# Kernel tuning notes

Measured on AMD Instinct MI355X. Metric: run time of the kernel, lower is better.

The kernel has to match this reference:

```python
import jax, jax.numpy as jnp
import numpy as np

N_HEADS = 16
DIM = 1024
HEAD_DIM = DIM // N_HEADS

def setup_inputs() -> dict:
    key = jax.random.key(0)
    ks = jax.random.split(key, 5)
    x = jax.random.normal(ks[0], (4, 2048, DIM), dtype=jnp.float32)
    W_attn = jax.random.normal(ks[1], (DIM, 3 * DIM), dtype=jnp.float32) / np.sqrt(DIM)
    b_attn = jnp.zeros((3 * DIM,), dtype=jnp.float32)
    W_proj = jax.random.normal(ks[2], (DIM, DIM), dtype=jnp.float32) / np.sqrt(DIM)
    b_proj = jnp.zeros((DIM,), dtype=jnp.float32)
    return {"x": x, "W_attn": W_attn, "b_attn": b_attn, "W_proj": W_proj, "b_proj": b_proj}

def reference(x, W_attn, b_attn, W_proj, b_proj):
    B, S, D = x.shape
    qkv = x @ W_attn + b_attn                      # [B,S,3D]
    q, k, v = jnp.split(qkv, 3, axis=2)
    def heads(t):
        return t.reshape(B, S, N_HEADS, HEAD_DIM).transpose(0, 2, 1, 3)  # [B,H,S,hd]
    qh, kh, vh = heads(q), heads(k), heads(v)
    scale = 1.0 / np.sqrt(HEAD_DIM).astype(np.float32)
    scores = jnp.einsum('bhqd,bhkd->bhqk', qh, kh) * scale  # [B,H,S,S]
    causal = jnp.tril(jnp.ones((S, S), dtype=bool))
    scores = jnp.where(causal, scores, -jnp.inf)
    probs = jax.nn.softmax(scores, axis=-1)
    ctx = jnp.einsum('bhqk,bhkd->bhqd', probs, vh)           # [B,H,S,hd]
    ctx = ctx.transpose(0, 2, 1, 3).reshape(B, S, D)
    return ctx @ W_proj + b_proj
```

## Files before the change

### kernel.cpp

```cpp
#include <hip/hip_runtime.h>
#include <hip/hip_bf16.h>
#include <stdint.h>

typedef __attribute__((ext_vector_type(4))) float  f32x4a;
typedef __attribute__((ext_vector_type(8))) short  bf16x8s;
typedef __attribute__((ext_vector_type(8))) unsigned short u16x8;

#define QSCALE 0.18033688011112042f

static __device__ __forceinline__ unsigned short f2bf(float f) {
    union { float f; uint32_t u; } v; v.f = f;
    uint32_t u = v.u;
    return (unsigned short)((u + 0x7FFFu + ((u >> 16) & 1u)) >> 16);
}

static __device__ __forceinline__ unsigned int pack2bf(float lo, float hi) {
    __hip_bfloat162 t = __float22bfloat162_rn(make_float2(lo, hi));
    union { __hip_bfloat162 b; unsigned int u; } c; c.b = t;
    return c.u;
}

static __device__ __forceinline__ float exp2a(float x) {
    float r;
    asm("v_exp_f32 %0, %1" : "=v"(r) : "v"(x));
    return r;
}

#define GLL(src, dst)                                                          \
    __builtin_amdgcn_global_load_lds(                                          \
        (const __attribute__((address_space(1))) void*)(src),                  \
        (__attribute__((address_space(3))) void*)(dst), 16, 0, 0)

__global__ __launch_bounds__(256) void k_cvt_bf16(const float* __restrict__ in,
                                                  unsigned short* __restrict__ out, int n8) {
    int i = blockIdx.x * blockDim.x + threadIdx.x;
    if (i >= n8) return;
    const float4* p = (const float4*)(in + (size_t)i * 8);
    float4 a = p[0], b = p[1];
    u16x8 o;
    o[0] = f2bf(a.x); o[1] = f2bf(a.y); o[2] = f2bf(a.z); o[3] = f2bf(a.w);
    o[4] = f2bf(b.x); o[5] = f2bf(b.y); o[6] = f2bf(b.z); o[7] = f2bf(b.w);
    *(u16x8*)(out + (size_t)i * 8) = o;
}

__global__ __launch_bounds__(256) void k_transpose_w(const float* __restrict__ W,
                                                     unsigned short* __restrict__ Wt,
                                                     int K, int N, float sc, int nscale) {
    __shared__ float tile[64][68];
    int bx = blockIdx.x;
    int ntn = N >> 6;
    int kt = bx / ntn, nt = bx % ntn;
    int t = threadIdx.x;
    int r0 = t >> 4;
    int c4 = (t & 15) << 2;
    for (int i = 0; i < 4; ++i) {
        int k = r0 + i * 16;
        float4 v = *(const float4*)(W + (size_t)(kt * 64 + k) * N + nt * 64 + c4);
        tile[k][c4 + 0] = v.x; tile[k][c4 + 1] = v.y;
        tile[k][c4 + 2] = v.z; tile[k][c4 + 3] = v.w;
    }
    __syncthreads();
    int nl = t >> 2;
    int kc = (t & 3) << 4;
    float s = (nt * 64 + nl < nscale) ? sc : 1.0f;
    unsigned short* dst = Wt + (size_t)(nt * 64 + nl) * K + kt * 64 + kc;
    u16x8 o0, o1;
    for (int i = 0; i < 8; ++i) o0[i] = f2bf(tile[kc + i][nl] * s);
    for (int i = 0; i < 8; ++i) o1[i] = f2bf(tile[kc + 8 + i][nl] * s);
    *(u16x8*)dst = o0;
    *(u16x8*)(dst + 8) = o1;
}

template<int OUT_BF16, int VW, int QS>
__global__ __launch_bounds__(512, 4) void k_gemm2b(const unsigned short* __restrict__ A,
                                                   const unsigned short* __restrict__ Bt,
                                                   const float* __restrict__ bias,
                                                   void* __restrict__ Cout,
                                                   unsigned short* __restrict__ vt,
                                                   int M, int N, int K, int ntn) {
    __shared__ __align__(16) unsigned short S[3][12288];
    unsigned short* Sf = &S[0][0];

    int nwg = gridDim.x;
    int bid = blockIdx.x;
    int wg = (bid & 7) * (nwg >> 3) + (bid >> 3);
    int mt = wg / ntn, nt = wg % ntn;
    size_t m0 = (size_t)mt * 128, n0 = (size_t)nt * 256;

    int tid = threadIdx.x;
    int w = tid >> 6, lane = tid & 63;
    int wm = w >> 2, wn = w & 3;
    int l15 = lane & 15, l4 = lane >> 4;

    int srow = tid >> 2;
    int sch = (tid & 3) ^ ((srow >> 1) & 3);
    const unsigned short* Asrc = A  + (m0 + srow) * (size_t)K + sch * 8;
    const unsigned short* Bsrc = Bt + (n0 + srow) * (size_t)K + sch * 8;

#define STG(bufoff, kt)                                                                   \
    do {                                                                                  \
        GLL(Asrc + (size_t)(kt) * 32,                    Sf + (bufoff) + tid * 8);        \
        GLL(Bsrc + (size_t)(kt) * 32,                    Sf + (bufoff) + 4096 + tid * 8); \
        GLL(Bsrc + (size_t)(kt) * 32 + (size_t)128 * K,  Sf + (bufoff) + 8192 + tid * 8); \
    } while (0)

    int ck = (l4 ^ ((l15 >> 1) & 3)) * 8;
    int aoff = (wm * 64 + l15) * 32 + ck;
    int boff = 4096 + (wn * 64 + l15) * 32 + ck;

    f32x4a acc[4][4] = {};

#define BAR() __builtin_amdgcn_s_barrier()

    int NT = K >> 5;

    STG(0, 0);
    STG(12288, 1);
    asm volatile("s_waitcnt vmcnt(3)" ::: "memory");
    __builtin_amdgcn_sched_barrier(0);
    BAR();

    int cb = 0;
    for (int t = 0; t < NT; ++t) {
        int sb = cb + 24576; if (sb >= 36864) sb -= 36864;
        bool more = (t + 2) < NT;
        if (more) STG(sb, t + 2);
        bf16x8s af[4], bf[4];
        #pragma unroll
        for (int q = 0; q < 4; ++q) af[q] = *(const bf16x8s*)(Sf + cb + aoff + q * 512);
        #pragma unroll
        for (int q = 0; q < 4; ++q) bf[q] = *(const bf16x8s*)(Sf + cb + boff + q * 512);
        #pragma unroll
        for (int mf = 0; mf < 4; ++mf)
            #pragma unroll
            for (int nf = 0; nf < 4; ++nf)
                acc[mf][nf] = __builtin_amdgcn_mfma_f32_16x16x32_bf16(af[mf], bf[nf],
                                                                      acc[mf][nf], 0, 0, 0);
        if (more) { asm volatile("s_waitcnt vmcnt(3)" ::: "memory"); }
        else      { asm volatile("s_waitcnt vmcnt(0)" ::: "memory"); }
        __builtin_amdgcn_sched_barrier(0);
        BAR();
        cb += 12288; if (cb >= 36864) cb = 0;
    }

    if (VW && nt >= 8) {
        int b = (int)(m0 >> 11);
        int sb_ = ((int)m0 & 2047) + wm * 64;
        #pragma unroll
        for (int nf = 0; nf < 4; ++nf) {
            int vc = ((int)n0 - 2048) + wn * 64 + nf * 16 + l15;
            int h = vc >> 6, d = vc & 63;
            float bv = bias[2048 + vc];
            unsigned short* vrow = vt + ((size_t)(b * 16 + h) * 64 + d) * 2048;
            #pragma unroll
            for (int mf = 0; mf < 4; ++mf) {
                int s = sb_ + mf * 16 + l4 * 4;
                uint2 pv = make_uint2(pack2bf(acc[mf][nf][0] + bv, acc[mf][nf][1] + bv),
                                      pack2bf(acc[mf][nf][2] + bv, acc[mf][nf][3] + bv));
                *(uint2*)(vrow + s) = pv;
            }
        }
    } else {
        #pragma unroll
        for (int nf = 0; nf < 4; ++nf) {
            int col = (int)n0 + wn * 64 + nf * 16 + l15;
            float bv = bias[col];
            if (QS && col < 1024) bv *= QSCALE;
            #pragma unroll
            for (int mf = 0; mf < 4; ++mf) {
                int rbase = (int)m0 + wm * 64 + mf * 16 + l4 * 4;
                #pragma unroll
                for (int rr = 0; rr < 4; ++rr) {
                    float v = acc[mf][nf][rr] + bv;
                    if (OUT_BF16)
                        ((unsigned short*)Cout)[(size_t)(rbase + rr) * N + col] = f2bf(v);
                    else
                        ((float*)Cout)[(size_t)(rbase + rr) * N + col] = v;
                }
            }
        }
    }
#undef STG
#undef BAR
}

__global__ __launch_bounds__(256, 2) void k_attn(const unsigned short* __restrict__ qkv,
                                                 const unsigned short* __restrict__ vt,
                                                 unsigned short* __restrict__ ctx) {
    __shared__ unsigned short Ks[2][8192];
    __shared__ unsigned short Vs[2][8192];
    __shared__ unsigned short Pb[4][2048];
    int bx = blockIdx.x;
    int bh = bx & 63;
    int pr = bx >> 6;
    int b = bh >> 4, hd = bh & 15;
    int tid = threadIdx.x;
    int w = tid >> 6, lane = tid & 63;
    int l15 = lane & 15, l4 = lane >> 4;

    const unsigned short* Qb  = qkv + (size_t)b * 2048 * 3072 + hd * 64;
    const unsigned short* Kb  = Qb + 1024;
    const unsigned short* Vtb = vt + (size_t)bh * 64 * 2048;

    int kr = tid >> 3, kc = tid & 7;
    const unsigned short* Ksr = Kb + (size_t)kr * 3072 + ((kc ^ (kr & 7)) << 3);
    int vr = tid >> 4, vc = tid & 15;
    const unsigned short* Vsr = Vtb + (size_t)vr * 2048 + ((vc ^ (vr & 7)) << 3);
    unsigned short* pbw = &Pb[w][0];

    int psw  = l15 & 7;
    int ph   = (l4 & 1) * 4;
    int pc0  = ((0 + (l4 >> 1)) ^ psw) * 8;
    int pc1  = ((2 + (l4 >> 1)) ^ psw) * 8;
    int pc2  = ((4 + (l4 >> 1)) ^ psw) * 8;
    int pc3  = ((6 + (l4 >> 1)) ^ psw) * 8;
    int pr0  = ((0 + l4) ^ psw) * 8;
    int pr1  = ((4 + l4) ^ psw) * 8;
    int prow0 = l15 * 64;
    int prow1 = (l15 + 16) * 64;

    bf16x8s onesf;
    #pragma unroll
    for (int i = 0; i < 8; ++i) onesf[i] = (short)0x3F80;

#define STAGE(buf, kv0s)                                                                 \
    do {                                                                                 \
        _Pragma("unroll")                                                                \
        for (int i_ = 0; i_ < 4; ++i_)                                                   \
            GLL(Ksr + (size_t)((kv0s) + 32 * i_) * 3072,                                 \
                &Ks[buf][i_ * 2048 + w * 512]);                                          \
        _Pragma("unroll")                                                                \
        for (int i_ = 0; i_ < 4; ++i_)                                                   \
            GLL(Vsr + (size_t)(16 * i_) * 2048 + (kv0s),                                 \
                &Vs[buf][i_ * 2048 + w * 512]);                                          \
    } while (0)

    for (int half = 0; half < 2; ++half) {
        int j = half ? (15 - pr) : pr;
        int q0 = j * 128 + w * 32;
        int qa0 = q0 + l15, qa1 = q0 + 16 + l15;
        bf16x8s qf[2][2];
        {
            const unsigned short* p0 = Qb + (size_t)(q0 + l15) * 3072 + l4 * 8;
            qf[0][0] = *(const bf16x8s*)p0;
            qf[0][1] = *(const bf16x8s*)(p0 + 32);
            const unsigned short* p1 = p0 + (size_t)16 * 3072;
            qf[1][0] = *(const bf16x8s*)p1;
            qf[1][1] = *(const bf16x8s*)(p1 + 32);
        }
        f32x4a o[2][4] = {};
        f32x4a lsum[2] = {};
        const int NT128 = j + 1;

        STAGE(0, 0);
        asm volatile("s_waitcnt vmcnt(0)" ::: "memory");
        __builtin_amdgcn_sched_barrier(0);
        __builtin_amdgcn_s_barrier();

        for (int t = 0; t < NT128; ++t) {
            int cur = t & 1;
            if (t + 1 < NT128) STAGE(cur ^ 1, (t + 1) * 128);

            const unsigned short* Kbuf = Ks[cur];
            const unsigned short* Vbuf = Vs[cur];

            #pragma unroll
            for (int hh2 = 0; hh2 < 2; ++hh2) {
                int kvh = t * 128 + hh2 * 64;
                if (kvh > q0 + 31) continue;

                bf16x8s vf[2][4];
                #pragma unroll
                for (int g = 0; g < 2; ++g)
                    #pragma unroll
                    for (int nf = 0; nf < 4; ++nf) {
                        int rv = nf * 16 + l15;
                        int c  = hh2 * 8 + g * 4 + l4;
                        vf[g][nf] = *(const bf16x8s*)(Vbuf + rv * 128 + ((c ^ (rv & 7)) << 3));
                    }

                f32x4a z[2][4];
                __builtin_amdgcn_s_setprio(1);
                #pragma unroll
                for (int f = 0; f < 4; ++f) {
                    int rk = hh2 * 64 + f * 16 + l15;
                    bf16x8s ka = *(const bf16x8s*)(Kbuf + rk * 64 + ((l4 ^ psw) << 3));
                    bf16x8s kb = *(const bf16x8s*)(Kbuf + rk * 64 + (((4 + l4) ^ psw) << 3));
                    #pragma unroll
                    for (int g = 0; g < 2; ++g) {
                        f32x4a zz = {0.f, 0.f, 0.f, 0.f};
                        zz = __builtin_amdgcn_mfma_f32_16x16x32_bf16(ka, qf[g][0], zz, 0, 0, 0);
                        zz = __builtin_amdgcn_mfma_f32_16x16x32_bf16(kb, qf[g][1], zz, 0, 0, 0);
                        z[g][f] = zz;
                    }
                }
                __builtin_amdgcn_s_setprio(0);

                if (kvh + 63 > q0) {
                    #pragma unroll
                    for (int f = 0; f < 4; ++f)
                        #pragma unroll
                        for (int r = 0; r < 4; ++r) {
                            int kvp = kvh + f * 16 + l4 * 4 + r;
                            if (kvp > qa0) z[0][f][r] = -1e30f;
                            if (kvp > qa1) z[1][f][r] = -1e30f;
                        }
                }

                f32x4a p4[2][4];
                #pragma unroll
                for (int g = 0; g < 2; ++g)
                    #pragma unroll
                    for (int f = 0; f < 4; ++f)
                        #pragma unroll
                        for (int r = 0; r < 4; ++r)
                            p4[g][f][r] = exp2a(z[g][f][r]);

                unsigned int pk[2][8];
                #pragma unroll
                for (int g = 0; g < 2; ++g)
                    #pragma unroll
                    for (int f = 0; f < 4; ++f) {
                        pk[g][2 * f]     = pack2bf(p4[g][f][0], p4[g][f][1]);
                        pk[g][2 * f + 1] = pack2bf(p4[g][f][2], p4[g][f][3]);
                    }

                *(uint2*)(pbw + prow0 + pc0 + ph) = make_uint2(pk[0][0], pk[0][1]);
                *(uint2*)(pbw + prow0 + pc1 + ph) = make_uint2(pk[0][2], pk[0][3]);
                *(uint2*)(pbw + prow0 + pc2 + ph) = make_uint2(pk[0][4], pk[0][5]);
                *(uint2*)(pbw + prow0 + pc3 + ph) = make_uint2(pk[0][6], pk[0][7]);
                *(uint2*)(pbw + prow1 + pc0 + ph) = make_uint2(pk[1][0], pk[1][1]);
                *(uint2*)(pbw + prow1 + pc1 + ph) = make_uint2(pk[1][2], pk[1][3]);
                *(uint2*)(pbw + prow1 + pc2 + ph) = make_uint2(pk[1][4], pk[1][5]);
                *(uint2*)(pbw + prow1 + pc3 + ph) = make_uint2(pk[1][6], pk[1][7]);
                asm volatile("" ::: "memory");
                bf16x8s pa[2][2];
                pa[0][0] = *(const bf16x8s*)(pbw + prow0 + pr0);
                pa[0][1] = *(const bf16x8s*)(pbw + prow0 + pr1);
                pa[1][0] = *(const bf16x8s*)(pbw + prow1 + pr0);
                pa[1][1] = *(const bf16x8s*)(pbw + prow1 + pr1);
                asm volatile("" ::: "memory");

                __builtin_amdgcn_s_setprio(1);
                #pragma unroll
                for (int hh = 0; hh < 2; ++hh)
                    #pragma unroll
                    for (int g = 0; g < 2; ++g) {
                        #pragma unroll
                        for (int nf = 0; nf < 4; ++nf)
                            o[g][nf] = __builtin_amdgcn_mfma_f32_16x16x32_bf16(
                                pa[g][hh], vf[hh][nf], o[g][nf], 0, 0, 0);
                        lsum[g] = __builtin_amdgcn_mfma_f32_16x16x32_bf16(
                            pa[g][hh], onesf, lsum[g], 0, 0, 0);
                    }
                __builtin_amdgcn_s_setprio(0);
            }

            asm volatile("s_waitcnt vmcnt(0)" ::: "memory");
            __builtin_amdgcn_sched_barrier(0);
            __builtin_amdgcn_s_barrier();
        }
        __syncthreads();

        float linv0[4], linv1[4];
        #pragma unroll
        for (int r = 0; r < 4; ++r) {
            linv0[r] = 1.0f / lsum[0][r];
            linv1[r] = 1.0f / lsum[1][r];
        }
        #pragma unroll
        for (int nf = 0; nf < 4; ++nf) {
            int col = hd * 64 + nf * 16 + l15;
            #pragma unroll
            for (int r = 0; r < 4; ++r) {
                int row0 = q0 + l4 * 4 + r;
                ctx[((size_t)b * 2048 + row0) * 1024 + col]      = f2bf(o[0][nf][r] * linv0[r]);
                ctx[((size_t)b * 2048 + row0 + 16) * 1024 + col] = f2bf(o[1][nf][r] * linv1[r]);
            }
        }
    }
#undef STAGE
}

extern "C" void kernel_launch(void* const* d_in, const int* in_sizes, int n_in,
                              void* d_out, int out_size, void* d_ws, size_t ws_size,
                              hipStream_t stream) {
    const float* x      = (const float*)d_in[0];
    const float* W_attn = (const float*)d_in[1];
    const float* b_attn = (const float*)d_in[2];
    const float* W_proj = (const float*)d_in[3];
    const float* b_proj = (const float*)d_in[4];

    char* ws = (char*)d_ws;
    unsigned short* xb  = (unsigned short*)ws; ws += (size_t)8192 * 1024 * 2;
    unsigned short* wta = (unsigned short*)ws; ws += (size_t)3072 * 1024 * 2;
    unsigned short* wtp = (unsigned short*)ws; ws += (size_t)1024 * 1024 * 2;
    unsigned short* qkv = (unsigned short*)ws; ws += (size_t)8192 * 3072 * 2;
    unsigned short* vt  = (unsigned short*)ws; ws += (size_t)64 * 64 * 2048 * 2;
    unsigned short* ctx = (unsigned short*)ws;

    k_cvt_bf16<<<4096, 256, 0, stream>>>(x, xb, 8192 * 1024 / 8);
    k_transpose_w<<<16 * 48, 256, 0, stream>>>(W_attn, wta, 1024, 3072, QSCALE, 1024);
    k_transpose_w<<<16 * 16, 256, 0, stream>>>(W_proj, wtp, 1024, 1024, 1.0f, 0);
    k_gemm2b<1, 1, 1><<<768, 512, 0, stream>>>(xb, wta, b_attn, (void*)qkv, vt, 8192, 3072, 1024, 12);
    k_attn<<<512, 256, 0, stream>>>(qkv, vt, ctx);
    k_gemm2b<0, 0, 0><<<256, 512, 0, stream>>>(ctx, wtp, b_proj, d_out, nullptr, 8192, 1024, 1024, 4);
}
```

Before: 154.4 us.

## Use smaller-tile triple-buffered GEMM for output projection to fill more CUs

Adds a new 128x128-tile GEMM kernel with 256 threads, a K-step of 32 and a three-stage LDS ring buffer using direct global-to-LDS loads. It replaces the previous 256-block launch of the larger-tile GEMM for the output projection with 512 blocks. The goal is better occupancy and CU coverage on the 8192x1024x1024 projection, which previously launched only 256 workgroups. In exchange, each block reuses less data, so global and L2 traffic per FLOP goes up.

```diff
diff --git a/kernel.cpp b/kernel.cpp
--- a/kernel.cpp
+++ b/kernel.cpp
@@ -184,6 +184,90 @@
 #undef BAR
 }
 
+__global__ __launch_bounds__(256, 4) void k_gemm_sm(const unsigned short* __restrict__ A,
+                                                    const unsigned short* __restrict__ Bt,
+                                                    const float* __restrict__ bias,
+                                                    float* __restrict__ Cout,
+                                                    int M, int N, int K, int ntn) {
+    __shared__ __align__(16) unsigned short S[3][8192];
+    unsigned short* Sf = &S[0][0];
+
+    int nwg = gridDim.x;
+    int bid = blockIdx.x;
+    int wg = (bid & 7) * (nwg >> 3) + (bid >> 3);
+    int mt = wg / ntn, nt = wg % ntn;
+    size_t m0 = (size_t)mt * 128, n0 = (size_t)nt * 128;
+
+    int tid = threadIdx.x;
+    int w = tid >> 6, lane = tid & 63;
+    int wm = w >> 1, wn = w & 1;
+    int l15 = lane & 15, l4 = lane >> 4;
+
+    int srow = tid >> 2;
+    int sch = (tid & 3) ^ ((srow >> 1) & 3);
+    const unsigned short* Asrc = A  + (m0 + srow) * (size_t)K + sch * 8;
+    const unsigned short* Bsrc = Bt + (n0 + srow) * (size_t)K + sch * 8;
+
+#define STGS(bufoff, kt)                                                                  \
+    do {                                                                                  \
+        GLL(Asrc + (size_t)(kt) * 32,                   Sf + (bufoff) + tid * 8);         \
+        GLL(Asrc + (size_t)(kt) * 32 + (size_t)64 * K,  Sf + (bufoff) + 2048 + tid * 8);  \
+        GLL(Bsrc + (size_t)(kt) * 32,                   Sf + (bufoff) + 4096 + tid * 8);  \
+        GLL(Bsrc + (size_t)(kt) * 32 + (size_t)64 * K,  Sf + (bufoff) + 6144 + tid * 8);  \
+    } while (0)
+
+    int ck = (l4 ^ ((l15 >> 1) & 3)) * 8;
+    int aoff = (wm * 64 + l15) * 32 + ck;
+    int boff = 4096 + (wn * 64 + l15) * 32 + ck;
+
+    f32x4a acc[4][4] = {};
+
+    int NT = K >> 5;
+
+    STGS(0, 0);
+    STGS(8192, 1);
+    asm volatile("s_waitcnt vmcnt(4)" ::: "memory");
+    __builtin_amdgcn_sched_barrier(0);
+    __builtin_amdgcn_s_barrier();
+
+    int cb = 0;
+    for (int t = 0; t < NT; ++t) {
+        int sb = cb + 16384; if (sb >= 24576) sb -= 24576;
+        bool more = (t + 2) < NT;
+        if (more) STGS(sb, t + 2);
+        bf16x8s af[4], bf[4];
+        #pragma unroll
+        for (int q = 0; q < 4; ++q) af[q] = *(const bf16x8s*)(Sf + cb + aoff + q * 512);
+        #pragma unroll
+        for (int q = 0; q < 4; ++q) bf[q] = *(const bf16x8s*)(Sf + cb + boff + q * 512);
+        #pragma unroll
+        for (int mf = 0; mf < 4; ++mf)
+            #pragma unroll
+            for (int nf = 0; nf < 4; ++nf)
+                acc[mf][nf] = __builtin_amdgcn_mfma_f32_16x16x32_bf16(af[mf], bf[nf],
+                                                                      acc[mf][nf], 0, 0, 0);
+        if (more) { asm volatile("s_waitcnt vmcnt(4)" ::: "memory"); }
+        else      { asm volatile("s_waitcnt vmcnt(0)" ::: "memory"); }
+        __builtin_amdgcn_sched_barrier(0);
+        __builtin_amdgcn_s_barrier();
+        cb += 8192; if (cb >= 24576) cb = 0;
+    }
+
+    #pragma unroll
+    for (int nf = 0; nf < 4; ++nf) {
+        int col = (int)n0 + wn * 64 + nf * 16 + l15;
+        float bv = bias[col];
+        #pragma unroll
+        for (int mf = 0; mf < 4; ++mf) {
+            int rbase = (int)m0 + wm * 64 + mf * 16 + l4 * 4;
+            #pragma unroll
+            for (int rr = 0; rr < 4; ++rr)
+                Cout[(size_t)(rbase + rr) * N + col] = acc[mf][nf][rr] + bv;
+        }
+    }
+#undef STGS
+}
+
 __global__ __launch_bounds__(256, 2) void k_attn(const unsigned short* __restrict__ qkv,
                                                  const unsigned short* __restrict__ vt,
                                                  unsigned short* __restrict__ ctx) {
@@ -404,5 +488,5 @@
     k_transpose_w<<<16 * 16, 256, 0, stream>>>(W_proj, wtp, 1024, 1024, 1.0f, 0);
     k_gemm2b<1, 1, 1><<<768, 512, 0, stream>>>(xb, wta, b_attn, (void*)qkv, vt, 8192, 3072, 1024, 12);
     k_attn<<<512, 256, 0, stream>>>(qkv, vt, ctx);
-    k_gemm2b<0, 0, 0><<<256, 512, 0, stream>>>(ctx, wtp, b_proj, d_out, nullptr, 8192, 1024, 1024, 4);
-}
+    k_gemm_sm<<<512, 256, 0, stream>>>(ctx, wtp, b_proj, (float*)d_out, 8192, 1024, 1024, 8);
+}
```

After: 155.0 us. About the same (+0.4%).

## Process both causal-paired query blocks in one shared KV sweep

Applied to the files above, without the earlier changes.

Instead of running two sequential passes over the KV tiles, one for query block pr and one for 15-pr, the workgroup now keeps both query blocks' Q fragments and accumulators live and sweeps the KV range of the longer block once. Each staged K/V tile is used by both blocks wherever causality allows. This removes the duplicate global-to-LDS loads and barriers for the shared prefix. The cost is doubled accumulator and Q register state, which raises register pressure and may lower occupancy or cause spills.

```diff
diff --git a/kernel.cpp b/kernel.cpp
--- a/kernel.cpp
+++ b/kernel.cpp
@@ -235,151 +235,156 @@
                 &Vs[buf][i_ * 2048 + w * 512]);                                          \
     } while (0)
 
-    for (int half = 0; half < 2; ++half) {
-        int j = half ? (15 - pr) : pr;
-        int q0 = j * 128 + w * 32;
-        int qa0 = q0 + l15, qa1 = q0 + 16 + l15;
-        bf16x8s qf[2][2];
-        {
-            const unsigned short* p0 = Qb + (size_t)(q0 + l15) * 3072 + l4 * 8;
-            qf[0][0] = *(const bf16x8s*)p0;
-            qf[0][1] = *(const bf16x8s*)(p0 + 32);
-            const unsigned short* p1 = p0 + (size_t)16 * 3072;
-            qf[1][0] = *(const bf16x8s*)p1;
-            qf[1][1] = *(const bf16x8s*)(p1 + 32);
+    int jA = pr, jB = 15 - pr;
+    int q0A = jA * 128 + w * 32, q0B = jB * 128 + w * 32;
+    int qa0A = q0A + l15, qa1A = q0A + 16 + l15;
+    int qa0B = q0B + l15, qa1B = q0B + 16 + l15;
+
+    bf16x8s qfA[2][2], qfB[2][2];
+    {
+        const unsigned short* pA0 = Qb + (size_t)(q0A + l15) * 3072 + l4 * 8;
+        qfA[0][0] = *(const bf16x8s*)pA0;
+        qfA[0][1] = *(const bf16x8s*)(pA0 + 32);
+        const unsigned short* pA1 = pA0 + (size_t)16 * 3072;
+        qfA[1][0] = *(const bf16x8s*)pA1;
+        qfA[1][1] = *(const bf16x8s*)(pA1 + 32);
+        const unsigned short* pB0 = Qb + (size_t)(q0B + l15) * 3072 + l4 * 8;
+        qfB[0][0] = *(const bf16x8s*)pB0;
+        qfB[0][1] = *(const bf16x8s*)(pB0 + 32);
+        const unsigned short* pB1 = pB0 + (size_t)16 * 3072;
+        qfB[1][0] = *(const bf16x8s*)pB1;
+        qfB[1][1] = *(const bf16x8s*)(pB1 + 32);
+    }
+    f32x4a oA[2][4] = {}, oB[2][4] = {};
+    f32x4a lsA[2] = {}, lsB[2] = {};
+    const int NT128 = jB + 1;
+
+#define BODY(QF, O, LS, Q0, QA0, QA1, kvh, hh2, Kbuf, Vbuf)                              \
+    do {                                                                                 \
+        bf16x8s vf[2][4];                                                                \
+        _Pragma("unroll")                                                                \
+        for (int g = 0; g < 2; ++g)                                                      \
+            _Pragma("unroll")                                                            \
+            for (int nf = 0; nf < 4; ++nf) {                                             \
+                int rv = nf * 16 + l15;                                                  \
+                int c  = (hh2) * 8 + g * 4 + l4;                                         \
+                vf[g][nf] = *(const bf16x8s*)((Vbuf) + rv * 128 + ((c ^ (rv & 7)) << 3));\
+            }                                                                            \
+        f32x4a z[2][4];                                                                  \
+        __builtin_amdgcn_s_setprio(1);                                                   \
+        _Pragma("unroll")                                                                \
+        for (int f = 0; f < 4; ++f) {                                                    \
+            int rk = (hh2) * 64 + f * 16 + l15;                                          \
+            bf16x8s ka = *(const bf16x8s*)((Kbuf) + rk * 64 + ((l4 ^ psw) << 3));        \
+            bf16x8s kb = *(const bf16x8s*)((Kbuf) + rk * 64 + (((4 + l4) ^ psw) << 3));  \
+            _Pragma("unroll")                                                            \
+            for (int g = 0; g < 2; ++g) {                                                \
+                f32x4a zz = {0.f, 0.f, 0.f, 0.f};                                        \
+                zz = __builtin_amdgcn_mfma_f32_16x16x32_bf16(ka, QF[g][0], zz, 0, 0, 0); \
+                zz = __builtin_amdgcn_mfma_f32_16x16x32_bf16(kb, QF[g][1], zz, 0, 0, 0); \
+                z[g][f] = zz;                                                            \
+            }                                                                            \
+        }                                                                                \
+        __builtin_amdgcn_s_setprio(0);                                                   \
+        if ((kvh) + 63 > (Q0)) {                                                         \
+            _Pragma("unroll")                                                            \
+            for (int f = 0; f < 4; ++f)                                                  \
+                _Pragma("unroll")                                                        \
+                for (int r = 0; r < 4; ++r) {                                            \
+                    int kvp = (kvh) + f * 16 + l4 * 4 + r;                               \
+                    if (kvp > (QA0)) z[0][f][r] = -1e30f;                                \
+                    if (kvp > (QA1)) z[1][f][r] = -1e30f;                                \
+                }                                                                        \
+        }                                                                                \
+        f32x4a p4[2][4];                                                                 \
+        _Pragma("unroll")                                                                \
+        for (int g = 0; g < 2; ++g)                                                      \
+            _Pragma("unroll")                                                            \
+            for (int f = 0; f < 4; ++f)                                                  \
+                _Pragma("unroll")                                                        \
+                for (int r = 0; r < 4; ++r)                                              \
+                    p4[g][f][r] = exp2a(z[g][f][r]);                                     \
+        unsigned int pk[2][8];                                                           \
+        _Pragma("unroll")                                                                \
+        for (int g = 0; g < 2; ++g)                                                      \
+            _Pragma("unroll")                                                            \
+            for (int f = 0; f < 4; ++f) {                                                \
+                pk[g][2 * f]     = pack2bf(p4[g][f][0], p4[g][f][1]);                    \
+                pk[g][2 * f + 1] = pack2bf(p4[g][f][2], p4[g][f][3]);                    \
+            }                                                                            \
+        *(uint2*)(pbw + prow0 + pc0 + ph) = make_uint2(pk[0][0], pk[0][1]);              \
+        *(uint2*)(pbw + prow0 + pc1 + ph) = make_uint2(pk[0][2], pk[0][3]);              \
+        *(uint2*)(pbw + prow0 + pc2 + ph) = make_uint2(pk[0][4], pk[0][5]);              \
+        *(uint2*)(pbw + prow0 + pc3 + ph) = make_uint2(pk[0][6], pk[0][7]);              \
+        *(uint2*)(pbw + prow1 + pc0 + ph) = make_uint2(pk[1][0], pk[1][1]);              \
+        *(uint2*)(pbw + prow1 + pc1 + ph) = make_uint2(pk[1][2], pk[1][3]);              \
+        *(uint2*)(pbw + prow1 + pc2 + ph) = make_uint2(pk[1][4], pk[1][5]);              \
+        *(uint2*)(pbw + prow1 + pc3 + ph) = make_uint2(pk[1][6], pk[1][7]);              \
+        asm volatile("" ::: "memory");                                                   \
+        bf16x8s pa[2][2];                                                                \
+        pa[0][0] = *(const bf16x8s*)(pbw + prow0 + pr0);                                 \
+        pa[0][1] = *(const bf16x8s*)(pbw + prow0 + pr1);                                 \
+        pa[1][0] = *(const bf16x8s*)(pbw + prow1 + pr0);                                 \
+        pa[1][1] = *(const bf16x8s*)(pbw + prow1 + pr1);                                 \
+        asm volatile("" ::: "memory");                                                   \
+        __builtin_amdgcn_s_setprio(1);                                                   \
+        _Pragma("unroll")                                                                \
+        for (int hh = 0; hh < 2; ++hh)                                                   \
+            _Pragma("unroll")                                                            \
+            for (int g = 0; g < 2; ++g) {                                                \
+                _Pragma("unroll")                                                        \
+                for (int nf = 0; nf < 4; ++nf)                                           \
+                    O[g][nf] = __builtin_amdgcn_mfma_f32_16x16x32_bf16(                  \
+                        pa[g][hh], vf[hh][nf], O[g][nf], 0, 0, 0);                       \
+                LS[g] = __builtin_amdgcn_mfma_f32_16x16x32_bf16(                         \
+                    pa[g][hh], onesf, LS[g], 0, 0, 0);                                   \
+            }                                                                            \
+        __builtin_amdgcn_s_setprio(0);                                                   \
+    } while (0)
+
+    STAGE(0, 0);
+    asm volatile("s_waitcnt vmcnt(0)" ::: "memory");
+    __builtin_amdgcn_sched_barrier(0);
+    __builtin_amdgcn_s_barrier();
+
+    for (int t = 0; t < NT128; ++t) {
+        int cur = t & 1;
+        if (t + 1 < NT128) STAGE(cur ^ 1, (t + 1) * 128);
+
+        const unsigned short* Kbuf = Ks[cur];
+        const unsigned short* Vbuf = Vs[cur];
+
+        #pragma unroll
+        for (int hh2 = 0; hh2 < 2; ++hh2) {
+            int kvh = t * 128 + hh2 * 64;
+            if (kvh <= q0B + 31)
+                BODY(qfB, oB, lsB, q0B, qa0B, qa1B, kvh, hh2, Kbuf, Vbuf);
+            if (kvh <= q0A + 31)
+                BODY(qfA, oA, lsA, q0A, qa0A, qa1A, kvh, hh2, Kbuf, Vbuf);
         }
-        f32x4a o[2][4] = {};
-        f32x4a lsum[2] = {};
-        const int NT128 = j + 1;
-
-        STAGE(0, 0);
+
         asm volatile("s_waitcnt vmcnt(0)" ::: "memory");
         __builtin_amdgcn_sched_barrier(0);
         __builtin_amdgcn_s_barrier();
-
-        for (int t = 0; t < NT128; ++t) {
-            int cur = t & 1;
-            if (t + 1 < NT128) STAGE(cur ^ 1, (t + 1) * 128);
-
-            const unsigned short* Kbuf = Ks[cur];
-            const unsigned short* Vbuf = Vs[cur];
-
-            #pragma unroll
-            for (int hh2 = 0; hh2 < 2; ++hh2) {
-                int kvh = t * 128 + hh2 * 64;
-                if (kvh > q0 + 31) continue;
-
-                bf16x8s vf[2][4];
-                #pragma unroll
-                for (int g = 0; g < 2; ++g)
-                    #pragma unroll
-                    for (int nf = 0; nf < 4; ++nf) {
-                        int rv = nf * 16 + l15;
-                        int c  = hh2 * 8 + g * 4 + l4;
-                        vf[g][nf] = *(const bf16x8s*)(Vbuf + rv * 128 + ((c ^ (rv & 7)) << 3));
-                    }
-
-                f32x4a z[2][4];
-                __builtin_amdgcn_s_setprio(1);
-                #pragma unroll
-                for (int f = 0; f < 4; ++f) {
-                    int rk = hh2 * 64 + f * 16 + l15;
-                    bf16x8s ka = *(const bf16x8s*)(Kbuf + rk * 64 + ((l4 ^ psw) << 3));
-                    bf16x8s kb = *(const bf16x8s*)(Kbuf + rk * 64 + (((4 + l4) ^ psw) << 3));
-                    #pragma unroll
-                    for (int g = 0; g < 2; ++g) {
-                        f32x4a zz = {0.f, 0.f, 0.f, 0.f};
-                        zz = __builtin_amdgcn_mfma_f32_16x16x32_bf16(ka, qf[g][0], zz, 0, 0, 0);
-                        zz = __builtin_amdgcn_mfma_f32_16x16x32_bf16(kb, qf[g][1], zz, 0, 0, 0);
-                        z[g][f] = zz;
-                    }
-                }
-                __builtin_amdgcn_s_setprio(0);
-
-                if (kvh + 63 > q0) {
-                    #pragma unroll
-                    for (int f = 0; f < 4; ++f)
-                        #pragma unroll
-                        for (int r = 0; r < 4; ++r) {
-                            int kvp = kvh + f * 16 + l4 * 4 + r;
-                            if (kvp > qa0) z[0][f][r] = -1e30f;
-                            if (kvp > qa1) z[1][f][r] = -1e30f;
-                        }
-                }
-
-                f32x4a p4[2][4];
-                #pragma unroll
-                for (int g = 0; g < 2; ++g)
-                    #pragma unroll
-                    for (int f = 0; f < 4; ++f)
-                        #pragma unroll
-                        for (int r = 0; r < 4; ++r)
-                            p4[g][f][r] = exp2a(z[g][f][r]);
-
-                unsigned int pk[2][8];
-                #pragma unroll
-                for (int g = 0; g < 2; ++g)
-                    #pragma unroll
-                    for (int f = 0; f < 4; ++f) {
-                        pk[g][2 * f]     = pack2bf(p4[g][f][0], p4[g][f][1]);
-                        pk[g][2 * f + 1] = pack2bf(p4[g][f][2], p4[g][f][3]);
-                    }
-
-                *(uint2*)(pbw + prow0 + pc0 + ph) = make_uint2(pk[0][0], pk[0][1]);
-                *(uint2*)(pbw + prow0 + pc1 + ph) = make_uint2(pk[0][2], pk[0][3]);
-                *(uint2*)(pbw + prow0 + pc2 + ph) = make_uint2(pk[0][4], pk[0][5]);
-                *(uint2*)(pbw + prow0 + pc3 + ph) = make_uint2(pk[0][6], pk[0][7]);
-                *(uint2*)(pbw + prow1 + pc0 + ph) = make_uint2(pk[1][0], pk[1][1]);
-                *(uint2*)(pbw + prow1 + pc1 + ph) = make_uint2(pk[1][2], pk[1][3]);
-                *(uint2*)(pbw + prow1 + pc2 + ph) = make_uint2(pk[1][4], pk[1][5]);
-                *(uint2*)(pbw + prow1 + pc3 + ph) = make_uint2(pk[1][6], pk[1][7]);
-                asm volatile("" ::: "memory");
-                bf16x8s pa[2][2];
-                pa[0][0] = *(const bf16x8s*)(pbw + prow0 + pr0);
-                pa[0][1] = *(const bf16x8s*)(pbw + prow0 + pr1);
-                pa[1][0] = *(const bf16x8s*)(pbw + prow1 + pr0);
-                pa[1][1] = *(const bf16x8s*)(pbw + prow1 + pr1);
-                asm volatile("" ::: "memory");
-
-                __builtin_amdgcn_s_setprio(1);
-                #pragma unroll
-                for (int hh = 0; hh < 2; ++hh)
-                    #pragma unroll
-                    for (int g = 0; g < 2; ++g) {
-                        #pragma unroll
-                        for (int nf = 0; nf < 4; ++nf)
-                            o[g][nf] = __builtin_amdgcn_mfma_f32_16x16x32_bf16(
-                                pa[g][hh], vf[hh][nf], o[g][nf], 0, 0, 0);
-                        lsum[g] = __builtin_amdgcn_mfma_f32_16x16x32_bf16(
-                            pa[g][hh], onesf, lsum[g], 0, 0, 0);
-                    }
-                __builtin_amdgcn_s_setprio(0);
-            }
-
-            asm volatile("s_waitcnt vmcnt(0)" ::: "memory");
-            __builtin_amdgcn_sched_barrier(0);
-            __builtin_amdgcn_s_barrier();
-        }
-        __syncthreads();
-
-        float linv0[4], linv1[4];
-        #pragma unroll
-        for (int r = 0; r < 4; ++r) {
-            linv0[r] = 1.0f / lsum[0][r];
-            linv1[r] = 1.0f / lsum[1][r];
-        }
+    }
+
+    #pragma unroll
+    for (int r = 0; r < 4; ++r) {
+        float liA0 = 1.0f / lsA[0][r], liA1 = 1.0f / lsA[1][r];
+        float liB0 = 1.0f / lsB[0][r], liB1 = 1.0f / lsB[1][r];
         #pragma unroll
         for (int nf = 0; nf < 4; ++nf) {
             int col = hd * 64 + nf * 16 + l15;
-            #pragma unroll
-            for (int r = 0; r < 4; ++r) {
-                int row0 = q0 + l4 * 4 + r;
-                ctx[((size_t)b * 2048 + row0) * 1024 + col]      = f2bf(o[0][nf][r] * linv0[r]);
-                ctx[((size_t)b * 2048 + row0 + 16) * 1024 + col] = f2bf(o[1][nf][r] * linv1[r]);
-            }
+            int rowA = q0A + l4 * 4 + r;
+            int rowB = q0B + l4 * 4 + r;
+            ctx[((size_t)b * 2048 + rowA) * 1024 + col]      = f2bf(oA[0][nf][r] * liA0);
+            ctx[((size_t)b * 2048 + rowA + 16) * 1024 + col] = f2bf(oA[1][nf][r] * liA1);
+            ctx[((size_t)b * 2048 + rowB) * 1024 + col]      = f2bf(oB[0][nf][r] * liB0);
+            ctx[((size_t)b * 2048 + rowB + 16) * 1024 + col] = f2bf(oB[1][nf][r] * liB1);
         }
     }
 #undef STAGE
+#undef BODY
 }
 
 extern "C" void kernel_launch(void* const* d_in, const int* in_sizes, int n_in,
```

Result: no change. 153.0 us, median of 2 (-0.9%).
